# Kernel optimization log

Measured on AMD Instinct MI355X. Metric: run time of the kernel, lower is better.

Reference implementation:

```python
import jax, jax.numpy as jnp
import numpy as np

N_NODES = 50000
N_EDGES = 800000
DIM_IN, DIM_H, DIM_OUT = 96, 128, 16


def setup_inputs() -> dict:
    key = jax.random.key(0)
    ks = jax.random.split(key, 8)
    x = jax.random.normal(ks[0], (N_NODES, DIM_IN), dtype=jnp.float32)
    edge_index = jax.random.randint(ks[1], (2, N_EDGES), 0, N_NODES, dtype=jnp.int64)
    W1_l = jax.random.normal(ks[2], (DIM_IN, DIM_H), dtype=jnp.float32) * 0.1
    b1_l = jax.random.normal(ks[3], (DIM_H,), dtype=jnp.float32) * 0.1
    W1_r = jax.random.normal(ks[4], (DIM_IN, DIM_H), dtype=jnp.float32) * 0.1
    W2_l = jax.random.normal(ks[5], (DIM_H, DIM_OUT), dtype=jnp.float32) * 0.1
    b2_l = jax.random.normal(ks[6], (DIM_OUT,), dtype=jnp.float32) * 0.1
    W2_r = jax.random.normal(ks[7], (DIM_H, DIM_OUT), dtype=jnp.float32) * 0.1
    return {"x": x, "edge_index": edge_index, "W1_l": W1_l, "b1_l": b1_l,
            "W1_r": W1_r, "W2_l": W2_l, "b2_l": b2_l, "W2_r": W2_r}


def _mean_aggregate(x, src, dst, n_nodes):
    # gather neighbor features along edges, mean-reduce at destination nodes
    msgs = x[src]                                      # [E, d]
    agg = jax.ops.segment_sum(msgs, dst, num_segments=n_nodes)  # [N, d]
    deg = jax.ops.segment_sum(jnp.ones_like(src, dtype=x.dtype), dst,
                              num_segments=n_nodes)    # [N]
    return agg / jnp.maximum(deg, 1.0)[:, None]


def _sage_conv(x, src, dst, W_l, b_l, W_r):
    # PyG SAGEConv (mean aggr): lin_l(mean_j x_j) + lin_r(x); bias on lin_l only
    agg = _mean_aggregate(x, src, dst, x.shape[0])
    return agg @ W_l + b_l + x @ W_r


def reference(x, edge_index, W1_l, b1_l, W1_r, W2_l, b2_l, W2_r):
    src, dst = edge_index[0], edge_index[1]
    h = jax.nn.relu(_sage_conv(x, src, dst, W1_l, b1_l, W1_r))
    h = _sage_conv(h, src, dst, W2_l, b2_l, W2_r)
    return jax.nn.softmax(h, axis=1)
```

## Files before the change

### kernel.cpp

```cpp
#include <hip/hip_runtime.h>

#define NN 50000
#define NE 800000
#define DIN 96
#define DH 128
#define DOUT 16
#define NBKT ((NN + 127) / 128)
#define CAPB 2560
#define EPB 8192
#define NSLC ((NE + EPB - 1) / EPB)
#define SLICE 52

typedef __attribute__((ext_vector_type(8))) short bf16x8;
typedef __attribute__((ext_vector_type(4))) float f32x4;
typedef unsigned short ushort_t;

__device__ inline short f2bf(float f) {
    unsigned u = __float_as_uint(f);
    u += 0x7fff + ((u >> 16) & 1);
    return (short)(u >> 16);
}
__device__ inline float bflo(unsigned u) { return __uint_as_float(u << 16); }
__device__ inline float bfhi(unsigned u) { return __uint_as_float(u & 0xffff0000u); }

#define XB_BLOCKS ((NN * DIN / 4 + 511) / 512)
#define WC_BLOCKS ((DH * 192 + 32 * DH + 511) / 512)
__global__ __launch_bounds__(512) void k_prep(const float* __restrict__ x,
                                              const float* __restrict__ W1l,
                                              const float* __restrict__ W1r,
                                              const float* __restrict__ W2l,
                                              const float* __restrict__ W2r,
                                              const int* __restrict__ ei,
                                              short* __restrict__ xb,
                                              short* __restrict__ Bt,
                                              short* __restrict__ Bt2,
                                              unsigned* __restrict__ bpack,
                                              int* __restrict__ scnt) {
    __shared__ unsigned stage[EPB];
    __shared__ int bcnt[NBKT];
    __shared__ int bfil[NBKT];
    __shared__ int brun[NBKT];
    __shared__ int sbuf[512];
    const int tid = threadIdx.x;

    if (blockIdx.x < XB_BLOCKS) {
        int i = blockIdx.x * 512 + tid;
        if (i < NN * DIN / 4) {
            float4 v = ((const float4*)x)[i];
            short4 o;
            o.x = f2bf(v.x); o.y = f2bf(v.y); o.z = f2bf(v.z); o.w = f2bf(v.w);
            ((short4*)xb)[i] = o;
        }
        return;
    }
    if (blockIdx.x < XB_BLOCKS + WC_BLOCKS) {
        int idx = (blockIdx.x - XB_BLOCKS) * 512 + tid;
        if (idx < DH * 192) {
            int n = idx / 192, kk = idx % 192;
            float v = (kk < DIN) ? W1l[kk * DH + n] : W1r[(kk - DIN) * DH + n];
            Bt[idx] = f2bf(v);
        } else if (idx < DH * 192 + 32 * DH) {
            int j = idx - DH * 192;
            int c = j >> 7, k = j & 127;
            float v = (c < DOUT) ? W2l[k * DOUT + c] : W2r[k * DOUT + (c - DOUT)];
            Bt2[j] = f2bf(v);
        }
        return;
    }
    const int j = blockIdx.x - XB_BLOCKS - WC_BLOCKS;
    const int e0 = j * EPB;
    const int ecnt = min(EPB, NE - e0);
    for (int i = tid; i < NBKT; i += 512) { bcnt[i] = 0; bfil[i] = 0; }
    __syncthreads();
    unsigned dcache[EPB / 512];
#pragma unroll
    for (int k = 0; k < EPB / 512; ++k) {
        int i = tid + k * 512;
        if (i < ecnt) {
            unsigned d = (unsigned)ei[NE + e0 + i];
            dcache[k] = d;
            atomicAdd(&bcnt[d >> 7], 1);
        }
    }
    __syncthreads();
    int v = (tid < NBKT) ? bcnt[tid] : 0;
    sbuf[tid] = v;
    __syncthreads();
    for (int o = 1; o < 512; o <<= 1) {
        int tv = (tid >= o) ? sbuf[tid - o] : 0;
        __syncthreads();
        sbuf[tid] += tv;
        __syncthreads();
    }
    if (tid < NBKT) brun[tid] = sbuf[tid] - v;
    __syncthreads();
#pragma unroll
    for (int k = 0; k < EPB / 512; ++k) {
        int i = tid + k * 512;
        if (i < ecnt) {
            unsigned s = (unsigned)ei[e0 + i];
            unsigned d = dcache[k];
            int b = d >> 7;
            int p = atomicAdd(&bfil[b], 1);
            stage[brun[b] + p] = (d << 16) | s;
        }
    }
    __syncthreads();
    for (int i = tid; i < ecnt; i += 512) {
        unsigned p = stage[i];
        int b = p >> 23;
        int idx = i - brun[b];
        if (idx < SLICE)
            bpack[((size_t)b * NSLC + j) * SLICE + idx] = p;
    }
    for (int b = tid; b < NBKT; b += 512)
        scnt[b * NSLC + j] = min(bcnt[b], SLICE);
}

__global__ __launch_bounds__(512) void k_mega(const short* __restrict__ xb,
                                              const unsigned* __restrict__ bpack,
                                              const int* __restrict__ scnt,
                                              const short* __restrict__ Bt,
                                              const float* __restrict__ b1,
                                              const short* __restrict__ Bt2,
                                              const float* __restrict__ b2,
                                              int* __restrict__ offs,
                                              int* __restrict__ offe,
                                              ushort_t* __restrict__ csr,
                                              short* __restrict__ zlb,
                                              float* __restrict__ sout) {
    __shared__ __align__(16) char uscr[128 * 136 * 2];
    unsigned* pairs = (unsigned*)uscr;
    short (*ht)[136] = (short(*)[136])uscr;
    __shared__ __align__(16) short m1t[128][104];
    __shared__ ushort_t csr_l[CAPB];
    __shared__ int scl[NSLC];
    __shared__ int sbs[NSLC];
    __shared__ int sbuf[512];
    __shared__ int ncnt[128];
    __shared__ int nrun[128];
    __shared__ int lcur[128];
    __shared__ float inv_l[128];
    __shared__ int cnt_s;

    const int b = blockIdx.x;
    const int tid = threadIdx.x;
    const int w = tid >> 6;
    const int l = tid & 63;

    if (tid < NSLC) scl[tid] = scnt[b * NSLC + tid];
    __syncthreads();
    int v = (tid < NSLC) ? scl[tid] : 0;
    sbuf[tid] = v;
    __syncthreads();
    for (int o = 1; o < 512; o <<= 1) {
        int tv = (tid >= o) ? sbuf[tid - o] : 0;
        __syncthreads();
        sbuf[tid] += tv;
        __syncthreads();
    }
    if (tid < NSLC) sbs[tid] = sbuf[tid] - v;
    if (tid == NSLC - 1) cnt_s = sbuf[tid];
    if (tid < 128) { ncnt[tid] = 0; lcur[tid] = 0; }
    __syncthreads();
    const int cnt = min(cnt_s, CAPB);

    for (int idx = tid; idx < NSLC * SLICE; idx += 512) {
        int j = idx / SLICE, k = idx - j * SLICE;
        if (k < scl[j]) {
            int pos = sbs[j] + k;
            if (pos < CAPB)
                pairs[pos] = bpack[((size_t)b * NSLC + j) * SLICE + k];
        }
    }
    __syncthreads();

    for (int i = tid; i < cnt; i += 512)
        atomicAdd(&ncnt[(pairs[i] >> 16) & 127], 1);
    __syncthreads();
    v = (tid < 128) ? ncnt[tid] : 0;
    sbuf[tid] = v;
    __syncthreads();
    for (int o = 1; o < 512; o <<= 1) {
        int tv = (tid >= o) ? sbuf[tid - o] : 0;
        __syncthreads();
        sbuf[tid] += tv;
        __syncthreads();
    }
    if (tid < 128) {
        nrun[tid] = sbuf[tid] - v;
        inv_l[tid] = v ? 1.0f / (float)v : 0.0f;
        const int n = b * 128 + tid;
        if (n < NN) {
            offs[n] = b * CAPB + nrun[tid];
            offe[n] = b * CAPB + nrun[tid] + v;
        }
    }
    __syncthreads();

    for (int i = tid; i < cnt; i += 512) {
        unsigned p = pairs[i];
        int nd = (p >> 16) & 127;
        int pos = atomicAdd(&lcur[nd], 1);
        csr_l[nrun[nd] + pos] = (ushort_t)(p & 0xffffu);
    }
    __syncthreads();

    for (int i = tid; i < CAPB / 2; i += 512)
        ((int*)csr)[(size_t)b * (CAPB / 2) + i] = ((const int*)csr_l)[i];

    {
        const int eg = l / 12;
        const int c  = l % 12;
        const float4* xq = (const float4*)xb;
        for (int nd = w; nd < 128; nd += 8) {
            const int bl = nrun[nd];
            const int deg = ncnt[nd];
            float acc[8];
#pragma unroll
            for (int k = 0; k < 8; ++k) acc[k] = 0.f;
            int i = (eg < 4) ? eg : deg;
            for (; i + 12 < deg; i += 16) {
                int s0 = csr_l[bl + i], s1 = csr_l[bl + i + 4];
                int s2 = csr_l[bl + i + 8], s3 = csr_l[bl + i + 12];
                float4 v0 = xq[(size_t)s0 * 12 + c];
                float4 v1 = xq[(size_t)s1 * 12 + c];
                float4 v2 = xq[(size_t)s2 * 12 + c];
                float4 v3 = xq[(size_t)s3 * 12 + c];
                const unsigned* u0 = (const unsigned*)&v0;
                const unsigned* u1 = (const unsigned*)&v1;
                const unsigned* u2 = (const unsigned*)&v2;
                const unsigned* u3 = (const unsigned*)&v3;
#pragma unroll
                for (int jj = 0; jj < 4; ++jj) {
                    acc[2 * jj]     += (bflo(u0[jj]) + bflo(u1[jj])) + (bflo(u2[jj]) + bflo(u3[jj]));
                    acc[2 * jj + 1] += (bfhi(u0[jj]) + bfhi(u1[jj])) + (bfhi(u2[jj]) + bfhi(u3[jj]));
                }
            }
            for (; i < deg; i += 4) {
                float4 v0 = xq[(size_t)csr_l[bl + i] * 12 + c];
                const unsigned* u0 = (const unsigned*)&v0;
#pragma unroll
                for (int jj = 0; jj < 4; ++jj) {
                    acc[2 * jj]     += bflo(u0[jj]);
                    acc[2 * jj + 1] += bfhi(u0[jj]);
                }
            }
#pragma unroll
            for (int k = 0; k < 8; ++k) acc[k] += __shfl(acc[k], l + 24);
#pragma unroll
            for (int k = 0; k < 8; ++k) acc[k] += __shfl(acc[k], l + 12);
            if (l < 12) {
                const float inv = inv_l[nd];
                uint4 o;
                unsigned* op = (unsigned*)&o;
#pragma unroll
                for (int jj = 0; jj < 4; ++jj)
                    op[jj] = (unsigned)(unsigned short)f2bf(acc[2 * jj] * inv)
                           | ((unsigned)(unsigned short)f2bf(acc[2 * jj + 1] * inv) << 16);
                *(uint4*)&m1t[nd][c * 8] = o;
            }
        }
    }
    __syncthreads();

    const int lr = l & 15;
    const int lk = l >> 4;
    int row_g = b * 128 + w * 16 + lr;
    if (row_g >= NN) row_g = NN - 1;

    f32x4 acc1[8];
#pragma unroll
    for (int nt = 0; nt < 8; ++nt) {
        float bv = b1[nt * 16 + lr];
        acc1[nt] = (f32x4){bv, bv, bv, bv};
    }
    bf16x8 afr[6];
    {
        const bf16x8* am = (const bf16x8*)&m1t[w * 16 + lr][0];
        const bf16x8* ax = (const bf16x8*)(xb + (size_t)row_g * DIN);
        afr[0] = am[lk];     afr[1] = am[4 + lk]; afr[2] = am[8 + lk];
        afr[3] = ax[lk];     afr[4] = ax[4 + lk]; afr[5] = ax[8 + lk];
    }
    const bf16x8* bt8 = (const bf16x8*)Bt;
#pragma unroll
    for (int st = 0; st < 6; ++st) {
#pragma unroll
        for (int nt = 0; nt < 8; ++nt) {
            bf16x8 bfr = bt8[(size_t)(nt * 16 + lr) * 24 + st * 4 + lk];
            acc1[nt] = __builtin_amdgcn_mfma_f32_16x16x32_bf16(afr[st], bfr, acc1[nt], 0, 0, 0);
        }
    }
    __syncthreads();
    const int lrow0 = w * 16 + lk * 4;
#pragma unroll
    for (int r = 0; r < 4; ++r) {
#pragma unroll
        for (int nt = 0; nt < 8; ++nt)
            ht[lrow0 + r][nt * 16 + lr] = f2bf(fmaxf(acc1[nt][r], 0.f));
    }
    __syncthreads();

    bf16x8 pafr[4];
#pragma unroll
    for (int st = 0; st < 4; ++st)
        pafr[st] = *(const bf16x8*)&ht[w * 16 + lr][st * 32 + lk * 8];

    f32x4 accz = (f32x4){0.f, 0.f, 0.f, 0.f};
    float bv = b2[lr];
    f32x4 accs = (f32x4){bv, bv, bv, bv};
    const bf16x8* b8 = (const bf16x8*)Bt2;
#pragma unroll
    for (int st = 0; st < 4; ++st) {
        bf16x8 bz = b8[(size_t)lr * 16 + st * 4 + lk];
        bf16x8 bs = b8[(size_t)(16 + lr) * 16 + st * 4 + lk];
        accz = __builtin_amdgcn_mfma_f32_16x16x32_bf16(pafr[st], bz, accz, 0, 0, 0);
        accs = __builtin_amdgcn_mfma_f32_16x16x32_bf16(pafr[st], bs, accs, 0, 0, 0);
    }
    const int orow0 = b * 128 + w * 16 + lk * 4;
#pragma unroll
    for (int r = 0; r < 4; ++r) {
        const int orow = orow0 + r;
        if (orow < NN) {
            zlb[(size_t)orow * DOUT + lr] = f2bf(accz[r]);
            sout[(size_t)orow * DOUT + lr] = accs[r];
        }
    }
}

__global__ __launch_bounds__(256) void k_agg2(const short* __restrict__ zlb,
                                              const float* __restrict__ s,
                                              const ushort_t* __restrict__ csr,
                                              const int* __restrict__ offs,
                                              const int* __restrict__ offe,
                                              float* __restrict__ out) {
    const int w = threadIdx.x >> 6;
    const int lane = threadIdx.x & 63;
    const int n = blockIdx.x * 4 + w;
    if (n >= NN) return;
    const int b = offs[n], e = offe[n];
    const int ng = lane >> 2;
    const int sl = lane & 3;
    const uint2* z2 = (const uint2*)zlb;
    float4 acc = {0.f, 0.f, 0.f, 0.f};
    for (int i = b + ng; i < e; i += 16) {
        uint2 u = z2[(size_t)csr[i] * 4 + sl];
        acc.x += bflo(u.x);
        acc.y += bfhi(u.x);
        acc.z += bflo(u.y);
        acc.w += bfhi(u.y);
    }
#pragma unroll
    for (int o = 4; o <= 32; o <<= 1) {
        acc.x += __shfl_xor(acc.x, o);
        acc.y += __shfl_xor(acc.y, o);
        acc.z += __shfl_xor(acc.z, o);
        acc.w += __shfl_xor(acc.w, o);
    }
    const float inv = (e > b) ? 1.0f / (float)(e - b) : 0.0f;
    const float4 sv = ((const float4*)s)[(size_t)n * 4 + sl];
    float4 v;
    v.x = acc.x * inv + sv.x;
    v.y = acc.y * inv + sv.y;
    v.z = acc.z * inv + sv.z;
    v.w = acc.w * inv + sv.w;
    float mx = fmaxf(fmaxf(v.x, v.y), fmaxf(v.z, v.w));
    mx = fmaxf(mx, __shfl_xor(mx, 1));
    mx = fmaxf(mx, __shfl_xor(mx, 2));
    v.x = expf(v.x - mx); v.y = expf(v.y - mx);
    v.z = expf(v.z - mx); v.w = expf(v.w - mx);
    float sm = v.x + v.y + v.z + v.w;
    sm += __shfl_xor(sm, 1);
    sm += __shfl_xor(sm, 2);
    const float r = 1.0f / sm;
    v.x *= r; v.y *= r; v.z *= r; v.w *= r;
    if (ng == 0) ((float4*)out)[(size_t)n * 4 + sl] = v;
}

template <typename T>
static inline T* align_up(void* p, size_t a = 64) {
    return (T*)(((uintptr_t)p + (a - 1)) & ~(uintptr_t)(a - 1));
}

extern "C" void kernel_launch(void* const* d_in, const int* in_sizes, int n_in,
                              void* d_out, int out_size, void* d_ws, size_t ws_size,
                              hipStream_t stream) {
    const float* x   = (const float*)d_in[0];
    const int*   ei  = (const int*)d_in[1];
    const float* W1l = (const float*)d_in[2];
    const float* b1  = (const float*)d_in[3];
    const float* W1r = (const float*)d_in[4];
    const float* W2l = (const float*)d_in[5];
    const float* b2  = (const float*)d_in[6];
    const float* W2r = (const float*)d_in[7];
    float* out = (float*)d_out;

    unsigned* bpack = (unsigned*)d_ws;
    int* scnt     = (int*)(bpack + (size_t)NBKT * NSLC * SLICE);
    float* s      = (float*)(scnt + (size_t)NBKT * NSLC);
    int* offs     = (int*)(s + (size_t)NN * DOUT);
    int* offe     = offs + NN;
    ushort_t* csr = (ushort_t*)align_up<short>(offe + NN);
    short* xb     = (short*)csr + (size_t)NBKT * CAPB;
    short* zlb    = xb + (size_t)NN * DIN;
    short* Bt     = zlb + (size_t)NN * DOUT;
    short* Bt2    = Bt + (size_t)DH * 192;

    k_prep<<<XB_BLOCKS + WC_BLOCKS + NSLC, 512, 0, stream>>>(
        x, W1l, W1r, W2l, W2r, ei, xb, Bt, Bt2, bpack, scnt);
    k_mega<<<NBKT, 512, 0, stream>>>(xb, bpack, scnt, Bt, b1, Bt2, b2,
                                     offs, offe, csr, zlb, s);
    k_agg2<<<(NN + 3) / 4, 256, 0, stream>>>(zlb, s, csr, offs, offe, out);
}
```

Before: 109.2 us.

## Split fused mega kernel into CSR build, aggregation and projection kernels

The single per-bucket kernel that built the local CSR, aggregated layer-1 neighbours and ran the MFMA projections is split into three kernels. A CSR-build kernel writes the CSR to global memory, a one-wavefront-per-node aggregation kernel writes the layer-1 means to a new bf16 buffer, and a 64-row projection kernel runs the GEMMs. The edge binning also uses smaller slices (2048 edges per slice, 24 slots) stored slice-major. The aim is to replace the low-occupancy, LDS-heavy megakernel with many small, well-occupied blocks, so gather parallelism and load balance across nodes improve. In exchange it adds two kernel launches, a global round trip for the aggregated features and the CSR, and a larger, more scattered bucket-pack read.

New measurement: 109.0 us. About the same (-0.2%).

```diff
diff --git a/kernel.cpp b/kernel.cpp
--- a/kernel.cpp
+++ b/kernel.cpp
@@ -7,9 +7,9 @@
 #define DOUT 16
 #define NBKT ((NN + 127) / 128)
 #define CAPB 2560
-#define EPB 8192
+#define EPB 2048
 #define NSLC ((NE + EPB - 1) / EPB)
-#define SLICE 52
+#define SLICE 24
 
 typedef __attribute__((ext_vector_type(8))) short bf16x8;
 typedef __attribute__((ext_vector_type(4))) float f32x4;
@@ -111,44 +111,30 @@
         int b = p >> 23;
         int idx = i - brun[b];
         if (idx < SLICE)
-            bpack[((size_t)b * NSLC + j) * SLICE + idx] = p;
+            bpack[((size_t)j * NBKT + b) * SLICE + idx] = p;
     }
     for (int b = tid; b < NBKT; b += 512)
-        scnt[b * NSLC + j] = min(bcnt[b], SLICE);
-}
-
-__global__ __launch_bounds__(512) void k_mega(const short* __restrict__ xb,
-                                              const unsigned* __restrict__ bpack,
-                                              const int* __restrict__ scnt,
-                                              const short* __restrict__ Bt,
-                                              const float* __restrict__ b1,
-                                              const short* __restrict__ Bt2,
-                                              const float* __restrict__ b2,
-                                              int* __restrict__ offs,
-                                              int* __restrict__ offe,
-                                              ushort_t* __restrict__ csr,
-                                              short* __restrict__ zlb,
-                                              float* __restrict__ sout) {
-    __shared__ __align__(16) char uscr[128 * 136 * 2];
-    unsigned* pairs = (unsigned*)uscr;
-    short (*ht)[136] = (short(*)[136])uscr;
-    __shared__ __align__(16) short m1t[128][104];
-    __shared__ ushort_t csr_l[CAPB];
+        scnt[j * NBKT + b] = min(bcnt[b], SLICE);
+}
+
+__global__ __launch_bounds__(512) void k_build(const unsigned* __restrict__ bpack,
+                                               const int* __restrict__ scnt,
+                                               int* __restrict__ offs,
+                                               int* __restrict__ offe,
+                                               ushort_t* __restrict__ csr) {
+    __shared__ unsigned pairs[CAPB];
     __shared__ int scl[NSLC];
     __shared__ int sbs[NSLC];
     __shared__ int sbuf[512];
     __shared__ int ncnt[128];
     __shared__ int nrun[128];
     __shared__ int lcur[128];
-    __shared__ float inv_l[128];
     __shared__ int cnt_s;
-
-    const int b = blockIdx.x;
+    const int bkt = blockIdx.x;
     const int tid = threadIdx.x;
-    const int w = tid >> 6;
-    const int l = tid & 63;
-
-    if (tid < NSLC) scl[tid] = scnt[b * NSLC + tid];
+
+    for (int j = tid; j < NSLC; j += 512) scl[j] = scnt[j * NBKT + bkt];
+    if (tid < 128) { ncnt[tid] = 0; lcur[tid] = 0; }
     __syncthreads();
     int v = (tid < NSLC) ? scl[tid] : 0;
     sbuf[tid] = v;
@@ -161,7 +147,6 @@
     }
     if (tid < NSLC) sbs[tid] = sbuf[tid] - v;
     if (tid == NSLC - 1) cnt_s = sbuf[tid];
-    if (tid < 128) { ncnt[tid] = 0; lcur[tid] = 0; }
     __syncthreads();
     const int cnt = min(cnt_s, CAPB);
 
@@ -170,7 +155,7 @@
         if (k < scl[j]) {
             int pos = sbs[j] + k;
             if (pos < CAPB)
-                pairs[pos] = bpack[((size_t)b * NSLC + j) * SLICE + k];
+                pairs[pos] = bpack[((size_t)j * NBKT + bkt) * SLICE + k];
         }
     }
     __syncthreads();
@@ -181,104 +166,114 @@
     v = (tid < 128) ? ncnt[tid] : 0;
     sbuf[tid] = v;
     __syncthreads();
-    for (int o = 1; o < 512; o <<= 1) {
-        int tv = (tid >= o) ? sbuf[tid - o] : 0;
-        __syncthreads();
-        sbuf[tid] += tv;
+    for (int o = 1; o < 128; o <<= 1) {
+        int tv = (tid >= o && tid < 128) ? sbuf[tid - o] : 0;
+        __syncthreads();
+        if (tid < 128) sbuf[tid] += tv;
         __syncthreads();
     }
     if (tid < 128) {
         nrun[tid] = sbuf[tid] - v;
-        inv_l[tid] = v ? 1.0f / (float)v : 0.0f;
-        const int n = b * 128 + tid;
+        const int n = bkt * 128 + tid;
         if (n < NN) {
-            offs[n] = b * CAPB + nrun[tid];
-            offe[n] = b * CAPB + nrun[tid] + v;
-        }
-    }
-    __syncthreads();
-
+            offs[n] = bkt * CAPB + nrun[tid];
+            offe[n] = bkt * CAPB + nrun[tid] + v;
+        }
+    }
+    __syncthreads();
     for (int i = tid; i < cnt; i += 512) {
         unsigned p = pairs[i];
         int nd = (p >> 16) & 127;
         int pos = atomicAdd(&lcur[nd], 1);
-        csr_l[nrun[nd] + pos] = (ushort_t)(p & 0xffffu);
-    }
-    __syncthreads();
-
-    for (int i = tid; i < CAPB / 2; i += 512)
-        ((int*)csr)[(size_t)b * (CAPB / 2) + i] = ((const int*)csr_l)[i];
-
-    {
-        const int eg = l / 12;
-        const int c  = l % 12;
-        const float4* xq = (const float4*)xb;
-        for (int nd = w; nd < 128; nd += 8) {
-            const int bl = nrun[nd];
-            const int deg = ncnt[nd];
-            float acc[8];
-#pragma unroll
-            for (int k = 0; k < 8; ++k) acc[k] = 0.f;
-            int i = (eg < 4) ? eg : deg;
-            for (; i + 12 < deg; i += 16) {
-                int s0 = csr_l[bl + i], s1 = csr_l[bl + i + 4];
-                int s2 = csr_l[bl + i + 8], s3 = csr_l[bl + i + 12];
-                float4 v0 = xq[(size_t)s0 * 12 + c];
-                float4 v1 = xq[(size_t)s1 * 12 + c];
-                float4 v2 = xq[(size_t)s2 * 12 + c];
-                float4 v3 = xq[(size_t)s3 * 12 + c];
-                const unsigned* u0 = (const unsigned*)&v0;
-                const unsigned* u1 = (const unsigned*)&v1;
-                const unsigned* u2 = (const unsigned*)&v2;
-                const unsigned* u3 = (const unsigned*)&v3;
-#pragma unroll
-                for (int jj = 0; jj < 4; ++jj) {
-                    acc[2 * jj]     += (bflo(u0[jj]) + bflo(u1[jj])) + (bflo(u2[jj]) + bflo(u3[jj]));
-                    acc[2 * jj + 1] += (bfhi(u0[jj]) + bfhi(u1[jj])) + (bfhi(u2[jj]) + bfhi(u3[jj]));
-                }
-            }
-            for (; i < deg; i += 4) {
-                float4 v0 = xq[(size_t)csr_l[bl + i] * 12 + c];
-                const unsigned* u0 = (const unsigned*)&v0;
-#pragma unroll
-                for (int jj = 0; jj < 4; ++jj) {
-                    acc[2 * jj]     += bflo(u0[jj]);
-                    acc[2 * jj + 1] += bfhi(u0[jj]);
-                }
-            }
-#pragma unroll
-            for (int k = 0; k < 8; ++k) acc[k] += __shfl(acc[k], l + 24);
-#pragma unroll
-            for (int k = 0; k < 8; ++k) acc[k] += __shfl(acc[k], l + 12);
-            if (l < 12) {
-                const float inv = inv_l[nd];
-                uint4 o;
-                unsigned* op = (unsigned*)&o;
-#pragma unroll
-                for (int jj = 0; jj < 4; ++jj)
-                    op[jj] = (unsigned)(unsigned short)f2bf(acc[2 * jj] * inv)
-                           | ((unsigned)(unsigned short)f2bf(acc[2 * jj + 1] * inv) << 16);
-                *(uint4*)&m1t[nd][c * 8] = o;
-            }
-        }
-    }
-    __syncthreads();
-
+        csr[(size_t)bkt * CAPB + nrun[nd] + pos] = (ushort_t)(p & 0xffffu);
+    }
+}
+
+__global__ __launch_bounds__(256) void k_agg1(const short* __restrict__ xb,
+                                              const ushort_t* __restrict__ csr,
+                                              const int* __restrict__ offs,
+                                              const int* __restrict__ offe,
+                                              short* __restrict__ m1b) {
+    const int w = threadIdx.x >> 6;
+    const int l = threadIdx.x & 63;
+    const int n = blockIdx.x * 4 + w;
+    if (n >= NN) return;
+    const int eg = l / 12;
+    const int c  = l % 12;
+    const int b = offs[n], e = offe[n];
+    const float4* xq = (const float4*)xb;
+    float acc[8];
+#pragma unroll
+    for (int k = 0; k < 8; ++k) acc[k] = 0.f;
+    int i = (eg < 4) ? b + eg : e;
+    for (; i + 12 < e; i += 16) {
+        int s0 = csr[i], s1 = csr[i + 4], s2 = csr[i + 8], s3 = csr[i + 12];
+        float4 v0 = xq[(size_t)s0 * 12 + c];
+        float4 v1 = xq[(size_t)s1 * 12 + c];
+        float4 v2 = xq[(size_t)s2 * 12 + c];
+        float4 v3 = xq[(size_t)s3 * 12 + c];
+        const unsigned* u0 = (const unsigned*)&v0;
+        const unsigned* u1 = (const unsigned*)&v1;
+        const unsigned* u2 = (const unsigned*)&v2;
+        const unsigned* u3 = (const unsigned*)&v3;
+#pragma unroll
+        for (int jj = 0; jj < 4; ++jj) {
+            acc[2 * jj]     += (bflo(u0[jj]) + bflo(u1[jj])) + (bflo(u2[jj]) + bflo(u3[jj]));
+            acc[2 * jj + 1] += (bfhi(u0[jj]) + bfhi(u1[jj])) + (bfhi(u2[jj]) + bfhi(u3[jj]));
+        }
+    }
+    for (; i < e; i += 4) {
+        float4 v0 = xq[(size_t)csr[i] * 12 + c];
+        const unsigned* u0 = (const unsigned*)&v0;
+#pragma unroll
+        for (int jj = 0; jj < 4; ++jj) {
+            acc[2 * jj]     += bflo(u0[jj]);
+            acc[2 * jj + 1] += bfhi(u0[jj]);
+        }
+    }
+#pragma unroll
+    for (int k = 0; k < 8; ++k) acc[k] += __shfl(acc[k], l + 24);
+#pragma unroll
+    for (int k = 0; k < 8; ++k) acc[k] += __shfl(acc[k], l + 12);
+    if (l < 12) {
+        const float inv = (e > b) ? 1.0f / (float)(e - b) : 0.0f;
+        uint4 o;
+        unsigned* op = (unsigned*)&o;
+#pragma unroll
+        for (int jj = 0; jj < 4; ++jj)
+            op[jj] = (unsigned)(unsigned short)f2bf(acc[2 * jj] * inv)
+                   | ((unsigned)(unsigned short)f2bf(acc[2 * jj + 1] * inv) << 16);
+        ((uint4*)m1b)[(size_t)n * 12 + l] = o;
+    }
+}
+
+#define SHP 136
+__global__ __launch_bounds__(256) void k_linproj(const short* __restrict__ m1b,
+                                                 const short* __restrict__ xb,
+                                                 const short* __restrict__ Bt,
+                                                 const float* __restrict__ b1,
+                                                 const short* __restrict__ Bt2,
+                                                 const float* __restrict__ b2,
+                                                 short* __restrict__ zlb,
+                                                 float* __restrict__ s) {
+    __shared__ __align__(16) short sh[64][SHP];
+    const int w = threadIdx.x >> 6;
+    const int l = threadIdx.x & 63;
     const int lr = l & 15;
     const int lk = l >> 4;
-    int row_g = b * 128 + w * 16 + lr;
-    if (row_g >= NN) row_g = NN - 1;
-
-    f32x4 acc1[8];
+    int row = blockIdx.x * 64 + w * 16 + lr;
+    if (row >= NN) row = NN - 1;
+
+    f32x4 acc[8];
 #pragma unroll
     for (int nt = 0; nt < 8; ++nt) {
         float bv = b1[nt * 16 + lr];
-        acc1[nt] = (f32x4){bv, bv, bv, bv};
+        acc[nt] = (f32x4){bv, bv, bv, bv};
     }
     bf16x8 afr[6];
     {
-        const bf16x8* am = (const bf16x8*)&m1t[w * 16 + lr][0];
-        const bf16x8* ax = (const bf16x8*)(xb + (size_t)row_g * DIN);
+        const bf16x8* am = (const bf16x8*)(m1b + (size_t)row * DIN);
+        const bf16x8* ax = (const bf16x8*)(xb  + (size_t)row * DIN);
         afr[0] = am[lk];     afr[1] = am[4 + lk]; afr[2] = am[8 + lk];
         afr[3] = ax[lk];     afr[4] = ax[4 + lk]; afr[5] = ax[8 + lk];
     }
@@ -288,23 +283,22 @@
 #pragma unroll
         for (int nt = 0; nt < 8; ++nt) {
             bf16x8 bfr = bt8[(size_t)(nt * 16 + lr) * 24 + st * 4 + lk];
-            acc1[nt] = __builtin_amdgcn_mfma_f32_16x16x32_bf16(afr[st], bfr, acc1[nt], 0, 0, 0);
-        }
-    }
-    __syncthreads();
+            acc[nt] = __builtin_amdgcn_mfma_f32_16x16x32_bf16(afr[st], bfr, acc[nt], 0, 0, 0);
+        }
+    }
     const int lrow0 = w * 16 + lk * 4;
 #pragma unroll
     for (int r = 0; r < 4; ++r) {
 #pragma unroll
         for (int nt = 0; nt < 8; ++nt)
-            ht[lrow0 + r][nt * 16 + lr] = f2bf(fmaxf(acc1[nt][r], 0.f));
+            sh[lrow0 + r][nt * 16 + lr] = f2bf(fmaxf(acc[nt][r], 0.f));
     }
     __syncthreads();
 
     bf16x8 pafr[4];
 #pragma unroll
     for (int st = 0; st < 4; ++st)
-        pafr[st] = *(const bf16x8*)&ht[w * 16 + lr][st * 32 + lk * 8];
+        pafr[st] = *(const bf16x8*)&sh[w * 16 + lr][st * 32 + lk * 8];
 
     f32x4 accz = (f32x4){0.f, 0.f, 0.f, 0.f};
     float bv = b2[lr];
@@ -317,13 +311,13 @@
         accz = __builtin_amdgcn_mfma_f32_16x16x32_bf16(pafr[st], bz, accz, 0, 0, 0);
         accs = __builtin_amdgcn_mfma_f32_16x16x32_bf16(pafr[st], bs, accs, 0, 0, 0);
     }
-    const int orow0 = b * 128 + w * 16 + lk * 4;
+    const int orow0 = blockIdx.x * 64 + w * 16 + lk * 4;
 #pragma unroll
     for (int r = 0; r < 4; ++r) {
         const int orow = orow0 + r;
         if (orow < NN) {
             zlb[(size_t)orow * DOUT + lr] = f2bf(accz[r]);
-            sout[(size_t)orow * DOUT + lr] = accs[r];
+            s[(size_t)orow * DOUT + lr] = accs[r];
         }
     }
 }
@@ -396,19 +390,21 @@
     float* out = (float*)d_out;
 
     unsigned* bpack = (unsigned*)d_ws;
-    int* scnt     = (int*)(bpack + (size_t)NBKT * NSLC * SLICE);
-    float* s      = (float*)(scnt + (size_t)NBKT * NSLC);
+    int* scnt     = (int*)(bpack + (size_t)NSLC * NBKT * SLICE);
+    float* s      = (float*)(scnt + (size_t)NSLC * NBKT);
     int* offs     = (int*)(s + (size_t)NN * DOUT);
     int* offe     = offs + NN;
     ushort_t* csr = (ushort_t*)align_up<short>(offe + NN);
     short* xb     = (short*)csr + (size_t)NBKT * CAPB;
-    short* zlb    = xb + (size_t)NN * DIN;
+    short* m1b    = xb + (size_t)NN * DIN;
+    short* zlb    = m1b + (size_t)NN * DIN;
     short* Bt     = zlb + (size_t)NN * DOUT;
     short* Bt2    = Bt + (size_t)DH * 192;
 
     k_prep<<<XB_BLOCKS + WC_BLOCKS + NSLC, 512, 0, stream>>>(
         x, W1l, W1r, W2l, W2r, ei, xb, Bt, Bt2, bpack, scnt);
-    k_mega<<<NBKT, 512, 0, stream>>>(xb, bpack, scnt, Bt, b1, Bt2, b2,
-                                     offs, offe, csr, zlb, s);
+    k_build<<<NBKT, 512, 0, stream>>>(bpack, scnt, offs, offe, csr);
+    k_agg1<<<(NN + 3) / 4, 256, 0, stream>>>(xb, csr, offs, offe, m1b);
+    k_linproj<<<(NN + 63) / 64, 256, 0, stream>>>(m1b, xb, Bt, b1, Bt2, b2, zlb, s);
     k_agg2<<<(NN + 3) / 4, 256, 0, stream>>>(zlb, s, csr, offs, offe, out);
 }
```

## Split each 128-node bucket across two 64-node blocks in the fused layer kernel

Applied to the files above, without the earlier changes.

The fused aggregation+GEMM kernel now runs 782 blocks of 64 destination nodes instead of 391 blocks of 128. Each block scans its parent bucket's packed edges and keeps only those whose destination falls in its half, using an atomic append instead of a prefix scan over slices. The goal is more blocks for better CU occupancy and less shared memory per block. In exchange, every edge slice is read twice, and only four of the eight waves do the MFMA stage. Edge order inside each node's CSR list now depends on atomic timing.

Measured after the change: 112.7 us. 3.3% more time.

```diff
diff --git a/kernel.cpp b/kernel.cpp
--- a/kernel.cpp
+++ b/kernel.cpp
@@ -5,11 +5,12 @@
 #define DIN 96
 #define DH 128
 #define DOUT 16
-#define NBKT ((NN + 127) / 128)
-#define CAPB 2560
+#define NBKT128 391
 #define EPB 8192
 #define NSLC ((NE + EPB - 1) / EPB)
 #define SLICE 52
+#define NBLK 782
+#define CAPB 1280
 
 typedef __attribute__((ext_vector_type(8))) short bf16x8;
 typedef __attribute__((ext_vector_type(4))) float f32x4;
@@ -37,9 +38,9 @@
                                               unsigned* __restrict__ bpack,
                                               int* __restrict__ scnt) {
     __shared__ unsigned stage[EPB];
-    __shared__ int bcnt[NBKT];
-    __shared__ int bfil[NBKT];
-    __shared__ int brun[NBKT];
+    __shared__ int bcnt[NBKT128];
+    __shared__ int bfil[NBKT128];
+    __shared__ int brun[NBKT128];
     __shared__ int sbuf[512];
     const int tid = threadIdx.x;
 
@@ -70,7 +71,7 @@
     const int j = blockIdx.x - XB_BLOCKS - WC_BLOCKS;
     const int e0 = j * EPB;
     const int ecnt = min(EPB, NE - e0);
-    for (int i = tid; i < NBKT; i += 512) { bcnt[i] = 0; bfil[i] = 0; }
+    for (int i = tid; i < NBKT128; i += 512) { bcnt[i] = 0; bfil[i] = 0; }
     __syncthreads();
     unsigned dcache[EPB / 512];
 #pragma unroll
@@ -83,7 +84,7 @@
         }
     }
     __syncthreads();
-    int v = (tid < NBKT) ? bcnt[tid] : 0;
+    int v = (tid < NBKT128) ? bcnt[tid] : 0;
     sbuf[tid] = v;
     __syncthreads();
     for (int o = 1; o < 512; o <<= 1) {
@@ -92,7 +93,7 @@
         sbuf[tid] += tv;
         __syncthreads();
     }
-    if (tid < NBKT) brun[tid] = sbuf[tid] - v;
+    if (tid < NBKT128) brun[tid] = sbuf[tid] - v;
     __syncthreads();
 #pragma unroll
     for (int k = 0; k < EPB / 512; ++k) {
@@ -113,107 +114,96 @@
         if (idx < SLICE)
             bpack[((size_t)b * NSLC + j) * SLICE + idx] = p;
     }
-    for (int b = tid; b < NBKT; b += 512)
+    for (int b = tid; b < NBKT128; b += 512)
         scnt[b * NSLC + j] = min(bcnt[b], SLICE);
 }
 
-__global__ __launch_bounds__(512) void k_mega(const short* __restrict__ xb,
-                                              const unsigned* __restrict__ bpack,
-                                              const int* __restrict__ scnt,
-                                              const short* __restrict__ Bt,
-                                              const float* __restrict__ b1,
-                                              const short* __restrict__ Bt2,
-                                              const float* __restrict__ b2,
-                                              int* __restrict__ offs,
-                                              int* __restrict__ offe,
-                                              ushort_t* __restrict__ csr,
-                                              short* __restrict__ zlb,
-                                              float* __restrict__ sout) {
-    __shared__ __align__(16) char uscr[128 * 136 * 2];
-    unsigned* pairs = (unsigned*)uscr;
-    short (*ht)[136] = (short(*)[136])uscr;
-    __shared__ __align__(16) short m1t[128][104];
+__global__ __launch_bounds__(512) void k_mega64(const short* __restrict__ xb,
+                                                const unsigned* __restrict__ bpack,
+                                                const int* __restrict__ scnt,
+                                                const short* __restrict__ Bt,
+                                                const float* __restrict__ b1,
+                                                const short* __restrict__ Bt2,
+                                                const float* __restrict__ b2,
+                                                int* __restrict__ offs,
+                                                int* __restrict__ offe,
+                                                ushort_t* __restrict__ csrg,
+                                                short* __restrict__ zlb,
+                                                float* __restrict__ sout) {
+    __shared__ __align__(16) short arena[64 * 136];
     __shared__ ushort_t csr_l[CAPB];
     __shared__ int scl[NSLC];
-    __shared__ int sbs[NSLC];
-    __shared__ int sbuf[512];
-    __shared__ int ncnt[128];
-    __shared__ int nrun[128];
-    __shared__ int lcur[128];
-    __shared__ float inv_l[128];
-    __shared__ int cnt_s;
-
-    const int b = blockIdx.x;
+    __shared__ int ncnt[64], nrun[64], lcur[64];
+    __shared__ float inv_l[64];
+    __shared__ int sbuf[64];
+    __shared__ int pcnt;
+
+    const int blk = blockIdx.x;
+    const int B = blk >> 1;
+    const unsigned half = blk & 1;
     const int tid = threadIdx.x;
     const int w = tid >> 6;
     const int l = tid & 63;
 
-    if (tid < NSLC) scl[tid] = scnt[b * NSLC + tid];
-    __syncthreads();
-    int v = (tid < NSLC) ? scl[tid] : 0;
-    sbuf[tid] = v;
-    __syncthreads();
-    for (int o = 1; o < 512; o <<= 1) {
-        int tv = (tid >= o) ? sbuf[tid - o] : 0;
-        __syncthreads();
-        sbuf[tid] += tv;
-        __syncthreads();
-    }
-    if (tid < NSLC) sbs[tid] = sbuf[tid] - v;
-    if (tid == NSLC - 1) cnt_s = sbuf[tid];
-    if (tid < 128) { ncnt[tid] = 0; lcur[tid] = 0; }
-    __syncthreads();
-    const int cnt = min(cnt_s, CAPB);
-
+    if (tid < NSLC) scl[tid] = scnt[B * NSLC + tid];
+    if (tid < 64) { ncnt[tid] = 0; lcur[tid] = 0; }
+    if (tid == 0) pcnt = 0;
+    __syncthreads();
+
+    unsigned* pairs = (unsigned*)arena;
+    const unsigned* bp = bpack + (size_t)B * NSLC * SLICE;
     for (int idx = tid; idx < NSLC * SLICE; idx += 512) {
         int j = idx / SLICE, k = idx - j * SLICE;
         if (k < scl[j]) {
-            int pos = sbs[j] + k;
-            if (pos < CAPB)
-                pairs[pos] = bpack[((size_t)b * NSLC + j) * SLICE + k];
-        }
-    }
-    __syncthreads();
+            unsigned p = bp[j * SLICE + k];
+            if (((p >> 22) & 1u) == half) {
+                int pos = atomicAdd(&pcnt, 1);
+                if (pos < CAPB) pairs[pos] = p;
+            }
+        }
+    }
+    __syncthreads();
+    const int cnt = min(pcnt, CAPB);
 
     for (int i = tid; i < cnt; i += 512)
-        atomicAdd(&ncnt[(pairs[i] >> 16) & 127], 1);
-    __syncthreads();
-    v = (tid < 128) ? ncnt[tid] : 0;
-    sbuf[tid] = v;
-    __syncthreads();
-    for (int o = 1; o < 512; o <<= 1) {
-        int tv = (tid >= o) ? sbuf[tid - o] : 0;
+        atomicAdd(&ncnt[(pairs[i] >> 16) & 63], 1);
+    __syncthreads();
+
+    if (tid < 64) sbuf[tid] = ncnt[tid];
+    __syncthreads();
+    for (int o = 1; o < 64; o <<= 1) {
+        int t = (tid < 64 && tid >= o) ? sbuf[tid - o] : 0;
         __syncthreads();
-        sbuf[tid] += tv;
+        if (tid < 64) sbuf[tid] += t;
         __syncthreads();
     }
-    if (tid < 128) {
-        nrun[tid] = sbuf[tid] - v;
-        inv_l[tid] = v ? 1.0f / (float)v : 0.0f;
-        const int n = b * 128 + tid;
+    if (tid < 64) {
+        nrun[tid] = sbuf[tid] - ncnt[tid];
+        inv_l[tid] = ncnt[tid] ? 1.0f / (float)ncnt[tid] : 0.0f;
+        const int n = blk * 64 + tid;
         if (n < NN) {
-            offs[n] = b * CAPB + nrun[tid];
-            offe[n] = b * CAPB + nrun[tid] + v;
-        }
-    }
-    __syncthreads();
-
+            offs[n] = blk * CAPB + nrun[tid];
+            offe[n] = blk * CAPB + nrun[tid] + ncnt[tid];
+        }
+    }
+    __syncthreads();
     for (int i = tid; i < cnt; i += 512) {
         unsigned p = pairs[i];
-        int nd = (p >> 16) & 127;
+        int nd = (p >> 16) & 63;
         int pos = atomicAdd(&lcur[nd], 1);
         csr_l[nrun[nd] + pos] = (ushort_t)(p & 0xffffu);
     }
     __syncthreads();
 
-    for (int i = tid; i < CAPB / 2; i += 512)
-        ((int*)csr)[(size_t)b * (CAPB / 2) + i] = ((const int*)csr_l)[i];
+    for (int i = tid; i < (cnt + 1) / 2; i += 512)
+        ((int*)csrg)[(size_t)blk * (CAPB / 2) + i] = ((const int*)csr_l)[i];
 
     {
+        short (*m1t)[104] = (short(*)[104])arena;
         const int eg = l / 12;
         const int c  = l % 12;
         const float4* xq = (const float4*)xb;
-        for (int nd = w; nd < 128; nd += 8) {
+        for (int nd = w * 8; nd < w * 8 + 8; ++nd) {
             const int bl = nrun[nd];
             const int deg = ncnt[nd];
             float acc[8];
@@ -266,64 +256,72 @@
 
     const int lr = l & 15;
     const int lk = l >> 4;
-    int row_g = b * 128 + w * 16 + lr;
-    if (row_g >= NN) row_g = NN - 1;
-
     f32x4 acc1[8];
-#pragma unroll
-    for (int nt = 0; nt < 8; ++nt) {
-        float bv = b1[nt * 16 + lr];
-        acc1[nt] = (f32x4){bv, bv, bv, bv};
-    }
-    bf16x8 afr[6];
-    {
-        const bf16x8* am = (const bf16x8*)&m1t[w * 16 + lr][0];
-        const bf16x8* ax = (const bf16x8*)(xb + (size_t)row_g * DIN);
-        afr[0] = am[lk];     afr[1] = am[4 + lk]; afr[2] = am[8 + lk];
-        afr[3] = ax[lk];     afr[4] = ax[4 + lk]; afr[5] = ax[8 + lk];
-    }
-    const bf16x8* bt8 = (const bf16x8*)Bt;
-#pragma unroll
-    for (int st = 0; st < 6; ++st) {
+    if (w < 4) {
+        short (*m1t)[104] = (short(*)[104])arena;
+        int row_g = blk * 64 + w * 16 + lr;
+        if (row_g >= NN) row_g = NN - 1;
 #pragma unroll
         for (int nt = 0; nt < 8; ++nt) {
-            bf16x8 bfr = bt8[(size_t)(nt * 16 + lr) * 24 + st * 4 + lk];
-            acc1[nt] = __builtin_amdgcn_mfma_f32_16x16x32_bf16(afr[st], bfr, acc1[nt], 0, 0, 0);
-        }
-    }
-    __syncthreads();
-    const int lrow0 = w * 16 + lk * 4;
-#pragma unroll
-    for (int r = 0; r < 4; ++r) {
-#pragma unroll
-        for (int nt = 0; nt < 8; ++nt)
-            ht[lrow0 + r][nt * 16 + lr] = f2bf(fmaxf(acc1[nt][r], 0.f));
-    }
-    __syncthreads();
-
-    bf16x8 pafr[4];
-#pragma unroll
-    for (int st = 0; st < 4; ++st)
-        pafr[st] = *(const bf16x8*)&ht[w * 16 + lr][st * 32 + lk * 8];
-
-    f32x4 accz = (f32x4){0.f, 0.f, 0.f, 0.f};
-    float bv = b2[lr];
-    f32x4 accs = (f32x4){bv, bv, bv, bv};
-    const bf16x8* b8 = (const bf16x8*)Bt2;
-#pragma unroll
-    for (int st = 0; st < 4; ++st) {
-        bf16x8 bz = b8[(size_t)lr * 16 + st * 4 + lk];
-        bf16x8 bs = b8[(size_t)(16 + lr) * 16 + st * 4 + lk];
-        accz = __builtin_amdgcn_mfma_f32_16x16x32_bf16(pafr[st], bz, accz, 0, 0, 0);
-        accs = __builtin_amdgcn_mfma_f32_16x16x32_bf16(pafr[st], bs, accs, 0, 0, 0);
-    }
-    const int orow0 = b * 128 + w * 16 + lk * 4;
-#pragma unroll
-    for (int r = 0; r < 4; ++r) {
-        const int orow = orow0 + r;
-        if (orow < NN) {
-            zlb[(size_t)orow * DOUT + lr] = f2bf(accz[r]);
-            sout[(size_t)orow * DOUT + lr] = accs[r];
+            float bv = b1[nt * 16 + lr];
+            acc1[nt] = (f32x4){bv, bv, bv, bv};
+        }
+        bf16x8 afr[6];
+        {
+            const bf16x8* am = (const bf16x8*)&m1t[w * 16 + lr][0];
+            const bf16x8* ax = (const bf16x8*)(xb + (size_t)row_g * DIN);
+            afr[0] = am[lk];     afr[1] = am[4 + lk]; afr[2] = am[8 + lk];
+            afr[3] = ax[lk];     afr[4] = ax[4 + lk]; afr[5] = ax[8 + lk];
+        }
+        const bf16x8* bt8 = (const bf16x8*)Bt;
+#pragma unroll
+        for (int st = 0; st < 6; ++st) {
+#pragma unroll
+            for (int nt = 0; nt < 8; ++nt) {
+                bf16x8 bfr = bt8[(size_t)(nt * 16 + lr) * 24 + st * 4 + lk];
+                acc1[nt] = __builtin_amdgcn_mfma_f32_16x16x32_bf16(afr[st], bfr, acc1[nt], 0, 0, 0);
+            }
+        }
+    }
+    __syncthreads();
+
+    short (*ht)[136] = (short(*)[136])arena;
+    if (w < 4) {
+        const int lrow0 = w * 16 + lk * 4;
+#pragma unroll
+        for (int r = 0; r < 4; ++r) {
+#pragma unroll
+            for (int nt = 0; nt < 8; ++nt)
+                ht[lrow0 + r][nt * 16 + lr] = f2bf(fmaxf(acc1[nt][r], 0.f));
+        }
+    }
+    __syncthreads();
+
+    if (w < 4) {
+        bf16x8 pafr[4];
+#pragma unroll
+        for (int st = 0; st < 4; ++st)
+            pafr[st] = *(const bf16x8*)&ht[w * 16 + lr][st * 32 + lk * 8];
+
+        f32x4 accz = (f32x4){0.f, 0.f, 0.f, 0.f};
+        float bv = b2[lr];
+        f32x4 accs = (f32x4){bv, bv, bv, bv};
+        const bf16x8* b8 = (const bf16x8*)Bt2;
+#pragma unroll
+        for (int st = 0; st < 4; ++st) {
+            bf16x8 bz = b8[(size_t)lr * 16 + st * 4 + lk];
+            bf16x8 bs = b8[(size_t)(16 + lr) * 16 + st * 4 + lk];
+            accz = __builtin_amdgcn_mfma_f32_16x16x32_bf16(pafr[st], bz, accz, 0, 0, 0);
+            accs = __builtin_amdgcn_mfma_f32_16x16x32_bf16(pafr[st], bs, accs, 0, 0, 0);
+        }
+        const int orow0 = blk * 64 + w * 16 + lk * 4;
+#pragma unroll
+        for (int r = 0; r < 4; ++r) {
+            const int orow = orow0 + r;
+            if (orow < NN) {
+                zlb[(size_t)orow * DOUT + lr] = f2bf(accz[r]);
+                sout[(size_t)orow * DOUT + lr] = accs[r];
+            }
         }
     }
 }
@@ -396,19 +394,19 @@
     float* out = (float*)d_out;
 
     unsigned* bpack = (unsigned*)d_ws;
-    int* scnt     = (int*)(bpack + (size_t)NBKT * NSLC * SLICE);
-    float* s      = (float*)(scnt + (size_t)NBKT * NSLC);
+    int* scnt     = (int*)(bpack + (size_t)NBKT128 * NSLC * SLICE);
+    float* s      = (float*)(scnt + (size_t)NBKT128 * NSLC);
     int* offs     = (int*)(s + (size_t)NN * DOUT);
     int* offe     = offs + NN;
     ushort_t* csr = (ushort_t*)align_up<short>(offe + NN);
-    short* xb     = (short*)csr + (size_t)NBKT * CAPB;
+    short* xb     = (short*)csr + (size_t)NBLK * CAPB;
     short* zlb    = xb + (size_t)NN * DIN;
     short* Bt     = zlb + (size_t)NN * DOUT;
     short* Bt2    = Bt + (size_t)DH * 192;
 
     k_prep<<<XB_BLOCKS + WC_BLOCKS + NSLC, 512, 0, stream>>>(
         x, W1l, W1r, W2l, W2r, ei, xb, Bt, Bt2, bpack, scnt);
-    k_mega<<<NBKT, 512, 0, stream>>>(xb, bpack, scnt, Bt, b1, Bt2, b2,
-                                     offs, offe, csr, zlb, s);
+    k_mega64<<<NBLK, 512, 0, stream>>>(xb, bpack, scnt, Bt, b1, Bt2, b2,
+                                       offs, offe, csr, zlb, s);
     k_agg2<<<(NN + 3) / 4, 256, 0, stream>>>(zlb, s, csr, offs, offe, out);
 }
```
